# Optimization experiments

Hardware: AMD Instinct MI355X
Metric: run time of the kernel (lower is better)

Reference implementation:

```python
import jax, jax.numpy as jnp
import numpy as np

B, D, E, H, C = 16384, 512, 16, 2048, 1
LN_EPS = 1e-5


def setup_inputs() -> dict:
    key = jax.random.key(0)
    ks = jax.random.split(key, 6)
    scale = 0.02
    return {
        "z": jax.random.normal(ks[0], (B, D), jnp.float32),
        "gate_w": jax.random.normal(ks[1], (D, E), jnp.float32) * scale,
        "gate_b": jnp.zeros((E,), jnp.float32),
        "ln_scale": jnp.ones((E, D), jnp.float32),
        "ln_bias": jnp.zeros((E, D), jnp.float32),
        "w1": jax.random.normal(ks[2], (E, D, H), jnp.float32) * scale,
        "b1": jnp.zeros((E, H), jnp.float32),
        "w2": jax.random.normal(ks[3], (E, H, C), jnp.float32) * scale,
        "b2": jnp.zeros((E, C), jnp.float32),
    }


def reference(z, gate_w, gate_b, ln_scale, ln_bias, w1, b1, w2, b2):
    # Gate: softmax over experts, top-1 routing by argmax
    g = jax.nn.softmax(z @ gate_w + gate_b, axis=-1)  # (B, E)
    idx = jnp.argmax(g, axis=-1)                      # (B,)

    # LayerNorm statistics are expert-independent (affine differs per expert)
    mu = jnp.mean(z, axis=-1, keepdims=True)
    var = jnp.mean(jnp.square(z - mu), axis=-1, keepdims=True)
    zn = (z - mu) / jnp.sqrt(var + LN_EPS)            # (B, D)

    # Loop over the small fixed expert set; combine by top-1 mask.
    logits = jnp.zeros((z.shape[0],), z.dtype)
    for e in range(E):
        x = zn * ln_scale[e] + ln_bias[e]                       # (B, D)
        h = jax.nn.gelu(x @ w1[e] + b1[e], approximate=False)   # (B, H)
        o = jnp.squeeze(h @ w2[e] + b2[e], axis=-1)             # (B,) since C==1
        logits = jnp.where(idx == e, o, logits)
    return logits, g
```

## Files before the change

### kernel.cpp

```cpp
#include <hip/hip_runtime.h>
#include <math.h>

#define NB 16384
#define ND 512
#define NE 16
#define NH 2048
#define BM 128
#define BN 128
#define BK 64
#define NCH (NH / BN)
#define NTB 2
#define LN_EPS 1e-5f

typedef __attribute__((ext_vector_type(8))) short s8v;
typedef __attribute__((ext_vector_type(4))) float f4v;

#define WS_W1T_OFF   ((size_t)0)
#define WS_W1T_BYTES ((size_t)NE * NH * ND * 2)
#define WS_XN_OFF    (WS_W1T_OFF + WS_W1T_BYTES)
#define WS_XN_BYTES  ((size_t)NB * ND * 2)
#define WS_XNS_OFF   (WS_XN_OFF + WS_XN_BYTES)
#define WS_XNS_BYTES ((size_t)NB * ND * 2)
#define WS_IDX_OFF   (WS_XNS_OFF + WS_XNS_BYTES)
#define WS_CNT_OFF   (WS_IDX_OFF + (size_t)NB * 4)
#define WS_ROWS_OFF  (WS_CNT_OFF + 256)

__device__ __forceinline__ unsigned short bf16_rne(float f) {
    unsigned u = __float_as_uint(f);
    unsigned r = (u + 0x7fffu + ((u >> 16) & 1u)) >> 16;
    return (unsigned short)r;
}

__global__ __launch_bounds__(256) void w1conv_kernel(
    const float* __restrict__ w1, unsigned short* __restrict__ w1t)
{
    int bid = blockIdx.x;
    int e = bid & 15;
    int rest = bid >> 4;
    int db = rest & 7;
    int hb = rest >> 3;
    int h = hb * 256 + threadIdx.x;

    const float* src = w1 + ((size_t)e * ND + db * 64) * NH + h;
    unsigned int u[32];
#pragma unroll
    for (int p = 0; p < 32; ++p) {
        float f0 = src[(size_t)(2 * p) * NH];
        float f1 = src[(size_t)(2 * p + 1) * NH];
        u[p] = (unsigned)bf16_rne(f0) | ((unsigned)bf16_rne(f1) << 16);
    }
    uint4* dst = reinterpret_cast<uint4*>(
        w1t + ((size_t)e * NH + h) * ND + db * 64);
#pragma unroll
    for (int p = 0; p < 8; ++p)
        dst[p] = make_uint4(u[4 * p], u[4 * p + 1], u[4 * p + 2], u[4 * p + 3]);
}

__global__ __launch_bounds__(256) void gate_ln_kernel(
    const float* __restrict__ z, const float* __restrict__ gw,
    const float* __restrict__ gb, const float* __restrict__ ln_s,
    const float* __restrict__ ln_b, const float* __restrict__ b2,
    unsigned short* __restrict__ xn, int* __restrict__ idx_ws,
    float* __restrict__ g_out, float* __restrict__ logits)
{
    int wave = threadIdx.x >> 6;
    int lane = threadIdx.x & 63;
    int b = blockIdx.x * 4 + wave;
    int q = lane & 3, dg = lane >> 2;

    const float* zr = z + (size_t)b * ND;
    float4 zv[8];
#pragma unroll
    for (int i = 0; i < 8; ++i)
        zv[i] = *reinterpret_cast<const float4*>(zr + dg * 32 + i * 4);

    float sum = 0.f, ssq = 0.f;
    float ga[4] = {0.f, 0.f, 0.f, 0.f};
#pragma unroll
    for (int i = 0; i < 8; ++i) {
        float zs[4] = {zv[i].x, zv[i].y, zv[i].z, zv[i].w};
#pragma unroll
        for (int t = 0; t < 4; ++t) {
            int d = dg * 32 + i * 4 + t;
            float4 w4 = *reinterpret_cast<const float4*>(gw + (size_t)d * NE + q * 4);
            ga[0] = fmaf(zs[t], w4.x, ga[0]);
            ga[1] = fmaf(zs[t], w4.y, ga[1]);
            ga[2] = fmaf(zs[t], w4.z, ga[2]);
            ga[3] = fmaf(zs[t], w4.w, ga[3]);
            sum += zs[t];
            ssq = fmaf(zs[t], zs[t], ssq);
        }
    }
#pragma unroll
    for (int m = 4; m <= 32; m <<= 1) {
        sum += __shfl_xor(sum, m);
        ssq += __shfl_xor(ssq, m);
#pragma unroll
        for (int j = 0; j < 4; ++j) ga[j] += __shfl_xor(ga[j], m);
    }
#pragma unroll
    for (int j = 0; j < 4; ++j) ga[j] += gb[q * 4 + j];

    float mu = sum * (1.f / ND);
    float var = ssq * (1.f / ND) - mu * mu;
    float rstd = rsqrtf(var + LN_EPS);

    float lmax = fmaxf(fmaxf(ga[0], ga[1]), fmaxf(ga[2], ga[3]));
    lmax = fmaxf(lmax, __shfl_xor(lmax, 1));
    lmax = fmaxf(lmax, __shfl_xor(lmax, 2));
    float ge[4], lsum = 0.f;
#pragma unroll
    for (int j = 0; j < 4; ++j) { ge[j] = __expf(ga[j] - lmax); lsum += ge[j]; }
    lsum += __shfl_xor(lsum, 1);
    lsum += __shfl_xor(lsum, 2);
    float rden = 1.f / lsum;

    int li = 1000;
#pragma unroll
    for (int j = 3; j >= 0; --j) if (ga[j] == lmax) li = q * 4 + j;
    li = min(li, __shfl_xor(li, 1));
    li = min(li, __shfl_xor(li, 2));

    float gv0 = ge[0] * rden, gv1 = ge[1] * rden;
    float gv2 = ge[2] * rden, gv3 = ge[3] * rden;
    int srcl = lane >> 2;
    float t0 = __shfl(gv0, srcl), t1 = __shfl(gv1, srcl);
    float t2 = __shfl(gv2, srcl), t3 = __shfl(gv3, srcl);
    float gval = (q == 0) ? t0 : (q == 1) ? t1 : (q == 2) ? t2 : t3;
    if (lane < NE) g_out[(size_t)b * NE + lane] = gval;

    float4 xa, xc;
    if (q == 0)      { xa = zv[0]; xc = zv[1]; }
    else if (q == 1) { xa = zv[2]; xc = zv[3]; }
    else if (q == 2) { xa = zv[4]; xc = zv[5]; }
    else             { xa = zv[6]; xc = zv[7]; }
    int dofs = dg * 32 + q * 8;
    const float* ls = ln_s + (size_t)li * ND + dofs;
    const float* lb = ln_b + (size_t)li * ND + dofs;
    float4 s0 = *reinterpret_cast<const float4*>(ls);
    float4 s1 = *reinterpret_cast<const float4*>(ls + 4);
    float4 u0 = *reinterpret_cast<const float4*>(lb);
    float4 u1 = *reinterpret_cast<const float4*>(lb + 4);
    unsigned short xb[8];
    xb[0] = bf16_rne((xa.x - mu) * rstd * s0.x + u0.x);
    xb[1] = bf16_rne((xa.y - mu) * rstd * s0.y + u0.y);
    xb[2] = bf16_rne((xa.z - mu) * rstd * s0.z + u0.z);
    xb[3] = bf16_rne((xa.w - mu) * rstd * s0.w + u0.w);
    xb[4] = bf16_rne((xc.x - mu) * rstd * s1.x + u1.x);
    xb[5] = bf16_rne((xc.y - mu) * rstd * s1.y + u1.y);
    xb[6] = bf16_rne((xc.z - mu) * rstd * s1.z + u1.z);
    xb[7] = bf16_rne((xc.w - mu) * rstd * s1.w + u1.w);
    *reinterpret_cast<s8v*>(xn + (size_t)b * ND + dofs) =
        *reinterpret_cast<s8v*>(xb);

    if (lane == 0) {
        idx_ws[b] = li;
        logits[b] = b2[li];
    }
}

__global__ __launch_bounds__(256) void bucket_kernel(
    const int* __restrict__ idx_ws, int* __restrict__ counts,
    int* __restrict__ rows)
{
    __shared__ int qc[4];
    int e = blockIdx.x;
    int tid = threadIdx.x, w = tid >> 6, lane = tid & 63;
    const int4* p = reinterpret_cast<const int4*>(idx_ws) + (size_t)w * 1024;

    int c = 0;
#pragma unroll 4
    for (int it = 0; it < 16; ++it) {
        int4 v = p[it * 64 + lane];
        c += (v.x == e) + (v.y == e) + (v.z == e) + (v.w == e);
    }
#pragma unroll
    for (int m = 1; m < 64; m <<= 1) c += __shfl_xor(c, m);
    if (lane == 0) qc[w] = c;
    __syncthreads();

    int base = 0;
    for (int j = 0; j < w; ++j) base += qc[j];
    unsigned long long below = (lane == 0) ? 0ull : ((~0ull) >> (64 - lane));
    int* re = rows + (size_t)e * NB;
    int run = base;
#pragma unroll 2
    for (int it = 0; it < 16; ++it) {
        int4 v = p[it * 64 + lane];
        int vv[4] = {v.x, v.y, v.z, v.w};
#pragma unroll
        for (int k = 0; k < 4; ++k) {
            unsigned long long m = __ballot(vv[k] == e);
            if (vv[k] == e)
                re[run + __popcll(m & below)] = w * 4096 + (it * 64 + lane) * 4 + k;
            run += __popcll(m);
        }
    }
    if (tid == 0) counts[e] = qc[0] + qc[1] + qc[2] + qc[3];
}

__global__ __launch_bounds__(256) void gather_kernel(
    const unsigned short* __restrict__ xn, const int* __restrict__ counts,
    const int* __restrict__ rows, unsigned short* __restrict__ xns)
{
    int wave = threadIdx.x >> 6, lane = threadIdx.x & 63;
    int slot = blockIdx.x * 4 + wave;

    int pfx = 0, e = 0;
#pragma unroll
    for (int i = 0; i < NE; ++i) {
        int c = counts[i];
        if (e == i && slot >= pfx + c) { pfx += c; e = i + 1; }
    }
    int row = rows[(size_t)e * NB + (slot - pfx)];
    s8v v = *reinterpret_cast<const s8v*>(xn + (size_t)row * ND + lane * 8);
    *reinterpret_cast<s8v*>(xns + (size_t)slot * ND + lane * 8) = v;
}

__global__ __launch_bounds__(256, 2) void mfma_mlp(
    const unsigned short* __restrict__ xns, const unsigned short* __restrict__ w1t,
    const float* __restrict__ b1, const float* __restrict__ w2,
    const int* __restrict__ counts, const int* __restrict__ rows,
    float* __restrict__ logits)
{
    __shared__ unsigned short A_lds[2][BM * BK];
    __shared__ unsigned short B_lds[2][BN * BK];

    int bid = blockIdx.x;
    int e = bid & 15;
    int rest = bid >> 4;
    int ch = rest & 15;
    int tb0 = rest >> 4;
    int c0 = ch * BN;
    int tid = threadIdx.x, lane = tid & 63, wave = tid >> 6;
    int wm = wave & 1, wn = wave >> 1;

    int cnt = counts[e];
    if (tb0 * BM >= cnt) return;
    int pfx = 0;
    for (int i = 0; i < e; ++i) pfx += counts[i];
    const int* rl = rows + (size_t)e * NB;

    int rquad = lane >> 3;
    int sbyte = ((lane & 7) * 16) ^ (rquad << 4);

    size_t boff[4];
#pragma unroll
    for (int i = 0; i < 4; ++i) {
        int cl = (wave * 4 + i) * 8 + rquad;
        boff[i] = ((size_t)(e * NH + c0 + cl) * ND) * 2 + sbyte;
    }

    float b1v[4], w2v[4];
#pragma unroll
    for (int cf = 0; cf < 4; ++cf) {
        int col = c0 + wn * 64 + cf * 16 + (lane & 15);
        b1v[cf] = b1[(size_t)e * NH + col];
        w2v[cf] = w2[(size_t)e * NH + col];
    }

    int g = lane >> 4;
    int fr = lane & 15;
    int sw = (lane & 7) << 4;
    int aoffs[4], boffs[4];
#pragma unroll
    for (int f = 0; f < 4; ++f) {
        aoffs[f] = (wm * 64 + f * 16 + fr) * 128;
        boffs[f] = (wn * 64 + f * 16 + fr) * 128;
    }

#define ISSUE_AB(buf, sbase, ss)                                             \
    {   _Pragma("unroll")                                                    \
        for (int i = 0; i < 4; ++i) {                                        \
            int rloc = (wave * 4 + i) * 8 + rquad;                           \
            int slot = min((sbase) + rloc, NB - 1);                          \
            __builtin_amdgcn_global_load_lds(                                \
                (const __attribute__((address_space(1))) void*)              \
                    ((const char*)xns + (size_t)slot * 1024 + (ss) * 128 + sbyte), \
                (__attribute__((address_space(3))) void*)                    \
                    &A_lds[buf][(wave * 4 + i) * 8 * BK], 16, 0, 0);         \
            __builtin_amdgcn_global_load_lds(                                \
                (const __attribute__((address_space(1))) void*)              \
                    ((const char*)w1t + boff[i] + (ss) * 128),               \
                (__attribute__((address_space(3))) void*)                    \
                    &B_lds[buf][(wave * 4 + i) * 8 * BK], 16, 0, 0); } }

    int tb = tb0;
    int sbase = pfx + tb * BM;

    ISSUE_AB(0, sbase, 0);

    while (true) {
        int tbn = tb + NTB;
        bool hasNext = (tbn * BM < cnt);
        int sbasen = pfx + tbn * BM;
        int rbase = tb * BM;

        f4v acc[4][4];
#pragma unroll
        for (int rf = 0; rf < 4; ++rf)
#pragma unroll
            for (int cf = 0; cf < 4; ++cf) acc[rf][cf] = (f4v){0.f, 0.f, 0.f, 0.f};

#pragma unroll
        for (int ss = 0; ss < 8; ++ss) {
            int cb = ss & 1;
            bool st = (ss < 7) || hasNext;
            int nss = (ss < 7) ? ss + 1 : 0;
            int nsb = (ss < 7) ? sbase : sbasen;

            __builtin_amdgcn_s_barrier();
            if (st) {
                ISSUE_AB(cb ^ 1, nsb, nss);
                asm volatile("s_waitcnt vmcnt(8)" ::: "memory");
            } else {
                asm volatile("s_waitcnt vmcnt(0)" ::: "memory");
            }
            __builtin_amdgcn_s_barrier();
            __builtin_amdgcn_sched_barrier(0);

#pragma unroll
            for (int ks = 0; ks < 2; ++ks) {
                int kb = (ks * 64 + g * 16) ^ sw;
                s8v a[4], bb[4];
#pragma unroll
                for (int rf = 0; rf < 4; ++rf)
                    a[rf] = *reinterpret_cast<const s8v*>(
                        (const char*)&A_lds[cb][0] + aoffs[rf] + kb);
#pragma unroll
                for (int cf = 0; cf < 4; ++cf)
                    bb[cf] = *reinterpret_cast<const s8v*>(
                        (const char*)&B_lds[cb][0] + boffs[cf] + kb);
#pragma unroll
                for (int rf = 0; rf < 4; ++rf)
#pragma unroll
                    for (int cf = 0; cf < 4; ++cf)
                        acc[rf][cf] = __builtin_amdgcn_mfma_f32_16x16x32_bf16(
                            a[rf], bb[cf], acc[rf][cf], 0, 0, 0);
            }
        }

#pragma unroll
        for (int rf = 0; rf < 4; ++rf) {
            float pj[4] = {0.f, 0.f, 0.f, 0.f};
#pragma unroll
            for (int cf = 0; cf < 4; ++cf) {
#pragma unroll
                for (int j = 0; j < 4; ++j) {
                    float h = acc[rf][cf][j] + b1v[cf];
                    float uu = h * (0.7978845608f + 0.0356774081f * h * h);
                    float ex = __expf(2.f * uu);
                    float th = 1.f - 2.f / (ex + 1.f);
                    pj[j] = fmaf(0.5f * h * (1.f + th), w2v[cf], pj[j]);
                }
            }
#pragma unroll
            for (int m = 1; m < 16; m <<= 1)
#pragma unroll
                for (int j = 0; j < 4; ++j) pj[j] += __shfl_xor(pj[j], m);
            if ((lane & 15) == 0) {
#pragma unroll
                for (int j = 0; j < 4; ++j) {
                    int rloc = wm * 64 + rf * 16 + g * 4 + j;
                    if (rbase + rloc < cnt)
                        atomicAdd(&logits[rl[rbase + rloc]], pj[j]);
                }
            }
        }

        if (!hasNext) break;
        tb = tbn;
        sbase = sbasen;
    }
#undef ISSUE_AB
}

extern "C" void kernel_launch(void* const* d_in, const int* in_sizes, int n_in,
                              void* d_out, int out_size, void* d_ws, size_t ws_size,
                              hipStream_t stream) {
    const float* z    = (const float*)d_in[0];
    const float* gw   = (const float*)d_in[1];
    const float* gb   = (const float*)d_in[2];
    const float* ln_s = (const float*)d_in[3];
    const float* ln_b = (const float*)d_in[4];
    const float* w1   = (const float*)d_in[5];
    const float* b1   = (const float*)d_in[6];
    const float* w2   = (const float*)d_in[7];
    const float* b2   = (const float*)d_in[8];

    float* logits = (float*)d_out;
    float* g_out  = (float*)d_out + NB;

    char* ws = (char*)d_ws;
    unsigned short* w1t = (unsigned short*)(ws + WS_W1T_OFF);
    unsigned short* xn  = (unsigned short*)(ws + WS_XN_OFF);
    unsigned short* xns = (unsigned short*)(ws + WS_XNS_OFF);
    int* idx_ws = (int*)(ws + WS_IDX_OFF);
    int* cnts   = (int*)(ws + WS_CNT_OFF);
    int* rowl   = (int*)(ws + WS_ROWS_OFF);

    w1conv_kernel<<<NE * 64, 256, 0, stream>>>(w1, w1t);
    gate_ln_kernel<<<NB / 4, 256, 0, stream>>>(z, gw, gb, ln_s, ln_b, b2,
                                               xn, idx_ws, g_out, logits);
    bucket_kernel<<<NE, 256, 0, stream>>>(idx_ws, cnts, rowl);
    gather_kernel<<<NB / 4, 256, 0, stream>>>(xn, cnts, rowl, xns);
    mfma_mlp<<<NE * NCH * NTB, 256, 0, stream>>>(xns, w1t, b1, w2, cnts, rowl,
                                                 logits);
}
```

Measured before the change: 175.1 us.

## Load GEMM operands directly from global memory instead of staging through LDS

Removes the double-buffered LDS staging (global_load_lds with swizzle, barriers, vmcnt waits) in the expert MLP GEMM. Each lane now reads its MFMA A and B fragments straight from global memory across 16 k-steps. This drops LDS usage and barrier synchronization, which may raise occupancy. In exchange each wave redundantly fetches the tiles it shares with other waves, and there is no software prefetch to hide global latency, so it leans on the L1/L2 caches.

```diff
diff --git a/kernel.cpp b/kernel.cpp
--- a/kernel.cpp
+++ b/kernel.cpp
@@ -7,7 +7,6 @@
 #define NH 2048
 #define BM 128
 #define BN 128
-#define BK 64
 #define NCH (NH / BN)
 #define NTB 2
 #define LN_EPS 1e-5f
@@ -223,9 +222,6 @@
     const int* __restrict__ counts, const int* __restrict__ rows,
     float* __restrict__ logits)
 {
-    __shared__ unsigned short A_lds[2][BM * BK];
-    __shared__ unsigned short B_lds[2][BN * BK];
-
     int bid = blockIdx.x;
     int e = bid & 15;
     int rest = bid >> 4;
@@ -241,60 +237,35 @@
     for (int i = 0; i < e; ++i) pfx += counts[i];
     const int* rl = rows + (size_t)e * NB;
 
-    int rquad = lane >> 3;
-    int sbyte = ((lane & 7) * 16) ^ (rquad << 4);
-
-    size_t boff[4];
-#pragma unroll
-    for (int i = 0; i < 4; ++i) {
-        int cl = (wave * 4 + i) * 8 + rquad;
-        boff[i] = ((size_t)(e * NH + c0 + cl) * ND) * 2 + sbyte;
+    int g8 = (lane >> 4) * 8;
+    int fr = lane & 15;
+
+    const unsigned short* bbase[4];
+#pragma unroll
+    for (int cf = 0; cf < 4; ++cf) {
+        int col = c0 + wn * 64 + cf * 16 + fr;
+        bbase[cf] = w1t + (size_t)(e * NH + col) * ND + g8;
     }
 
     float b1v[4], w2v[4];
 #pragma unroll
     for (int cf = 0; cf < 4; ++cf) {
-        int col = c0 + wn * 64 + cf * 16 + (lane & 15);
+        int col = c0 + wn * 64 + cf * 16 + fr;
         b1v[cf] = b1[(size_t)e * NH + col];
         w2v[cf] = w2[(size_t)e * NH + col];
     }
-
     int g = lane >> 4;
-    int fr = lane & 15;
-    int sw = (lane & 7) << 4;
-    int aoffs[4], boffs[4];
-#pragma unroll
-    for (int f = 0; f < 4; ++f) {
-        aoffs[f] = (wm * 64 + f * 16 + fr) * 128;
-        boffs[f] = (wn * 64 + f * 16 + fr) * 128;
-    }
-
-#define ISSUE_AB(buf, sbase, ss)                                             \
-    {   _Pragma("unroll")                                                    \
-        for (int i = 0; i < 4; ++i) {                                        \
-            int rloc = (wave * 4 + i) * 8 + rquad;                           \
-            int slot = min((sbase) + rloc, NB - 1);                          \
-            __builtin_amdgcn_global_load_lds(                                \
-                (const __attribute__((address_space(1))) void*)              \
-                    ((const char*)xns + (size_t)slot * 1024 + (ss) * 128 + sbyte), \
-                (__attribute__((address_space(3))) void*)                    \
-                    &A_lds[buf][(wave * 4 + i) * 8 * BK], 16, 0, 0);         \
-            __builtin_amdgcn_global_load_lds(                                \
-                (const __attribute__((address_space(1))) void*)              \
-                    ((const char*)w1t + boff[i] + (ss) * 128),               \
-                (__attribute__((address_space(3))) void*)                    \
-                    &B_lds[buf][(wave * 4 + i) * 8 * BK], 16, 0, 0); } }
-
-    int tb = tb0;
-    int sbase = pfx + tb * BM;
-
-    ISSUE_AB(0, sbase, 0);
-
-    while (true) {
-        int tbn = tb + NTB;
-        bool hasNext = (tbn * BM < cnt);
-        int sbasen = pfx + tbn * BM;
+
+    for (int tb = tb0; tb * BM < cnt; tb += NTB) {
         int rbase = tb * BM;
+        int sbase = pfx + rbase;
+
+        const unsigned short* abase[4];
+#pragma unroll
+        for (int rf = 0; rf < 4; ++rf) {
+            int slot = min(sbase + wm * 64 + rf * 16 + fr, NB - 1);
+            abase[rf] = xns + (size_t)slot * ND + g8;
+        }
 
         f4v acc[4][4];
 #pragma unroll
@@ -303,41 +274,20 @@
             for (int cf = 0; cf < 4; ++cf) acc[rf][cf] = (f4v){0.f, 0.f, 0.f, 0.f};
 
 #pragma unroll
-        for (int ss = 0; ss < 8; ++ss) {
-            int cb = ss & 1;
-            bool st = (ss < 7) || hasNext;
-            int nss = (ss < 7) ? ss + 1 : 0;
-            int nsb = (ss < 7) ? sbase : sbasen;
-
-            __builtin_amdgcn_s_barrier();
-            if (st) {
-                ISSUE_AB(cb ^ 1, nsb, nss);
-                asm volatile("s_waitcnt vmcnt(8)" ::: "memory");
-            } else {
-                asm volatile("s_waitcnt vmcnt(0)" ::: "memory");
-            }
-            __builtin_amdgcn_s_barrier();
-            __builtin_amdgcn_sched_barrier(0);
-
-#pragma unroll
-            for (int ks = 0; ks < 2; ++ks) {
-                int kb = (ks * 64 + g * 16) ^ sw;
-                s8v a[4], bb[4];
-#pragma unroll
-                for (int rf = 0; rf < 4; ++rf)
-                    a[rf] = *reinterpret_cast<const s8v*>(
-                        (const char*)&A_lds[cb][0] + aoffs[rf] + kb);
+        for (int ks = 0; ks < 16; ++ks) {
+            s8v a[4], b[4];
+#pragma unroll
+            for (int rf = 0; rf < 4; ++rf)
+                a[rf] = *reinterpret_cast<const s8v*>(abase[rf] + ks * 32);
+#pragma unroll
+            for (int cf = 0; cf < 4; ++cf)
+                b[cf] = *reinterpret_cast<const s8v*>(bbase[cf] + ks * 32);
+#pragma unroll
+            for (int rf = 0; rf < 4; ++rf)
 #pragma unroll
                 for (int cf = 0; cf < 4; ++cf)
-                    bb[cf] = *reinterpret_cast<const s8v*>(
-                        (const char*)&B_lds[cb][0] + boffs[cf] + kb);
-#pragma unroll
-                for (int rf = 0; rf < 4; ++rf)
-#pragma unroll
-                    for (int cf = 0; cf < 4; ++cf)
-                        acc[rf][cf] = __builtin_amdgcn_mfma_f32_16x16x32_bf16(
-                            a[rf], bb[cf], acc[rf][cf], 0, 0, 0);
-            }
+                    acc[rf][cf] = __builtin_amdgcn_mfma_f32_16x16x32_bf16(
+                        a[rf], b[cf], acc[rf][cf], 0, 0, 0);
         }
 
 #pragma unroll
@@ -367,12 +317,7 @@
                 }
             }
         }
-
-        if (!hasNext) break;
-        tb = tbn;
-        sbase = sbasen;
-    }
-#undef ISSUE_AB
+    }
 }
 
 extern "C" void kernel_launch(void* const* d_in, const int* in_sizes, int n_in,
```

New measurement: 256.2 us. 1.46x slower.
